# Optimization experiments

Hardware: AMD Instinct MI355X
Metric: run time of the kernel (lower is better)

The kernel has to match this reference:

```python
import math
import jax, jax.numpy as jnp
import numpy as np

D_MODEL = 1024
HEADS = 16
B, S = 4, 2048


def setup_inputs() -> dict:
    key = jax.random.key(0)
    ks = jax.random.split(key, 8)
    scale = 1.0 / math.sqrt(D_MODEL)
    return {
        "q": jax.random.normal(ks[0], (B, S, D_MODEL), dtype=jnp.float32),
        "k": jax.random.normal(ks[1], (B, S, D_MODEL), dtype=jnp.float32),
        "v": jax.random.normal(ks[2], (B, S, D_MODEL), dtype=jnp.float32),
        "mask": jax.random.randint(ks[3], (B, S), 0, 2).astype(jnp.bool_),
        "alibi_mask": jax.random.normal(ks[4], (1, HEADS, S, S), dtype=jnp.float32),
        "Wq": jax.random.normal(ks[5], (D_MODEL, D_MODEL), dtype=jnp.float32) * scale,
        "Wk": jax.random.normal(ks[6], (D_MODEL, D_MODEL), dtype=jnp.float32) * scale,
        "Wv": jax.random.normal(ks[7], (D_MODEL, D_MODEL), dtype=jnp.float32) * scale,
    }


def _split_heads(x):
    b, s, d = x.shape
    return x.reshape(b, s, HEADS, d // HEADS).transpose(0, 2, 1, 3)  # [B,H,S,hd]


def reference(q, k, v, mask, alibi_mask, Wq, Wk, Wv):
    # QKV projections (Linear, no bias)
    qh = _split_heads(q @ Wq)
    kh = _split_heads(k @ Wk)
    vh = _split_heads(v @ Wv)
    depth = qh.shape[-1]
    # naive full attention matrix [B,H,Sq,Sk]
    w = jnp.einsum("bhqd,bhkd->bhqk", qh, kh) / math.sqrt(depth)
    # mask: [B,Sk] -> [B,1,1,Sk], True = masked
    w = jnp.where(mask[:, None, None, :], -jnp.inf, w)
    w = w + alibi_mask
    a = jax.nn.softmax(w, axis=-1)  # dropout p=0 -> identity
    out = jnp.einsum("bhqk,bhkd->bhqd", a, vh)
    # combine heads -> [B,S,D]
    out = out.transpose(0, 2, 1, 3).reshape(q.shape[0], q.shape[1], -1)
    return (out, a)
```

## Files before the change

kernel.cpp:

```cpp
#include <hip/hip_runtime.h>
#include <hip/hip_bf16.h>
#include <math.h>

constexpr int B  = 4;
constexpr int S  = 2048;
constexpr int D  = 1024;
constexpr int H  = 16;
constexpr int HD = 64;
constexpr float SCALE = 0.125f;

using f32x4 = __attribute__((ext_vector_type(4))) float;
using s16x8 = __attribute__((ext_vector_type(8))) short;
using u16x8 = __attribute__((ext_vector_type(8))) unsigned short;
using u16x4 = __attribute__((ext_vector_type(4))) unsigned short;

__device__ __forceinline__ unsigned short f2bf(float f) {
    union { float f; unsigned u; } x; x.f = f;
    unsigned r = x.u + 0x7fffu + ((x.u >> 16) & 1u);
    return (unsigned short)(r >> 16);
}
__device__ __forceinline__ float bf2f(unsigned short h) {
    union { unsigned u; float f; } x; x.u = ((unsigned)h) << 16;
    return x.f;
}

#define MFMA_BF16(Af, Bf, Cf) __builtin_amdgcn_mfma_f32_16x16x32_bf16(Af, Bf, Cf, 0, 0, 0)

__global__ __launch_bounds__(256) void k_wt(const float* __restrict__ W,
                                            unsigned short* __restrict__ Wt) {
    __shared__ unsigned short T[64][68];
    const int k0 = blockIdx.x * 64, n0 = blockIdx.y * 64;
    const int t = threadIdx.x;
    {
        const int kr = t >> 4, nc4 = (t & 15) * 4;
        for (int rr = 0; rr < 4; ++rr) {
            const int kk = kr + rr * 16;
            f32x4 wv = *reinterpret_cast<const f32x4*>(&W[(size_t)(k0 + kk) * D + n0 + nc4]);
#pragma unroll
            for (int j = 0; j < 4; ++j) T[nc4 + j][kk] = f2bf(wv[j]);
        }
    }
    __syncthreads();
    {
        const int nr = t >> 4, kc4 = (t & 15) * 4;
        for (int rr = 0; rr < 4; ++rr) {
            const int nn = nr + rr * 16;
            u16x4 o;
#pragma unroll
            for (int j = 0; j < 4; ++j) o[j] = T[nn][kc4 + j];
            *reinterpret_cast<u16x4*>(&Wt[(size_t)(n0 + nn) * D + k0 + kc4]) = o;
        }
    }
}

__global__ __launch_bounds__(256) void k_proj_mfma(const float* __restrict__ X,
                                                   const unsigned short* __restrict__ Wt,
                                                   unsigned short* __restrict__ Y) {
    __shared__ alignas(16) unsigned short As[128][72];
    __shared__ alignas(16) unsigned short Bs[128][72];
    const int bm = blockIdx.y * 128, bn = blockIdx.x * 128;
    const int t = threadIdx.x, w = t >> 6, l = t & 63;
    const int wr = w >> 1, wc = w & 1;
    const int lr = l & 15, lg = l >> 4;
    f32x4 acc[4][4] = {};

    for (int k0 = 0; k0 < D; k0 += 64) {
        {
            const int c4 = (t & 15) * 4;
            int row = t >> 4;
            for (int rr = 0; rr < 8; ++rr, row += 16) {
                f32x4 xv = *reinterpret_cast<const f32x4*>(&X[(size_t)(bm + row) * D + k0 + c4]);
                u16x4 hv;
#pragma unroll
                for (int j = 0; j < 4; ++j) hv[j] = f2bf(xv[j]);
                *reinterpret_cast<u16x4*>(&As[row][c4]) = hv;
            }
        }
        for (int i = 0; i < 4; ++i) {
            const int idx = t + i * 256;
            const int row = idx >> 3, c8 = (idx & 7) * 8;
            *reinterpret_cast<u16x8*>(&Bs[row][c8]) =
                *reinterpret_cast<const u16x8*>(&Wt[(size_t)(bn + row) * D + k0 + c8]);
        }
        __syncthreads();
#pragma unroll
        for (int kk = 0; kk < 2; ++kk) {
            s16x8 af[4], bf[4];
#pragma unroll
            for (int f = 0; f < 4; ++f) {
                af[f] = *reinterpret_cast<const s16x8*>(&As[wr * 64 + f * 16 + lr][kk * 32 + lg * 8]);
                bf[f] = *reinterpret_cast<const s16x8*>(&Bs[wc * 64 + f * 16 + lr][kk * 32 + lg * 8]);
            }
#pragma unroll
            for (int fm = 0; fm < 4; ++fm)
#pragma unroll
                for (int fn = 0; fn < 4; ++fn)
                    acc[fm][fn] = MFMA_BF16(af[fm], bf[fn], acc[fm][fn]);
        }
        __syncthreads();
    }
#pragma unroll
    for (int fm = 0; fm < 4; ++fm)
#pragma unroll
        for (int fn = 0; fn < 4; ++fn)
#pragma unroll
            for (int r = 0; r < 4; ++r) {
                const int m = bm + wr * 64 + fm * 16 + lg * 4 + r;
                const int n = bn + wc * 64 + fn * 16 + lr;
                const int b = m >> 11, s = m & (S - 1);
                const int h = n >> 6, e = n & 63;
                Y[(((size_t)(b * H + h) * S) + s) * HD + e] = f2bf(acc[fm][fn][r]);
            }
}

__global__ __launch_bounds__(256) void k_vt(const unsigned short* __restrict__ Vh,
                                            unsigned short* __restrict__ VT) {
    __shared__ alignas(16) unsigned short T[64][264];
    const int bh = blockIdx.y;
    const int s0 = blockIdx.x * 256;
    const int t = threadIdx.x;
    {
        const int e4 = (t & 15) * 4;
        int sr = t >> 4;
        for (int rr = 0; rr < 16; ++rr, sr += 16) {
            u16x4 vv = *reinterpret_cast<const u16x4*>(&Vh[((size_t)bh * S + s0 + sr) * HD + e4]);
#pragma unroll
            for (int j = 0; j < 4; ++j) T[e4 + j][sr] = vv[j];
        }
    }
    __syncthreads();
    {
        const int e = t >> 2, sl0 = (t & 3) * 64;
        for (int c = 0; c < 8; ++c) {
            u16x8 o = *reinterpret_cast<const u16x8*>(&T[e][sl0 + c * 8]);
            *reinterpret_cast<u16x8*>(&VT[((size_t)bh * HD + e) * S + s0 + sl0 + c * 8]) = o;
        }
    }
}

__global__ __launch_bounds__(256) void k_abf16(const float* __restrict__ A,
                                               unsigned short* __restrict__ O) {
    const size_t N = (size_t)H * S * S;
    const size_t stride = (size_t)gridDim.x * 256 * 8;
    for (size_t i = ((size_t)blockIdx.x * 256 + threadIdx.x) * 8; i < N; i += stride) {
        f32x4 a0 = *reinterpret_cast<const f32x4*>(&A[i]);
        f32x4 a1 = *reinterpret_cast<const f32x4*>(&A[i + 4]);
        u16x8 o;
#pragma unroll
        for (int j = 0; j < 4; ++j) { o[j] = f2bf(a0[j]); o[4 + j] = f2bf(a1[j]); }
        *reinterpret_cast<u16x8*>(&O[i]) = o;
    }
}

template <bool ABF16>
__global__ __launch_bounds__(512, 4) void k_sumexp(
    const unsigned short* __restrict__ QH, const unsigned short* __restrict__ KH,
    const float* __restrict__ ALIBI, const unsigned short* __restrict__ ABF,
    const int* __restrict__ MASK, float* __restrict__ INVL) {
    __shared__ alignas(16) unsigned short Ks[64][72];
    __shared__ alignas(16) unsigned short ALs[128][72];

    const int bh = blockIdx.y, b = bh >> 4, h = bh & 15;
    const int q0 = blockIdx.x * 128;
    const int t = threadIdx.x, w = t >> 6, ln = t & 63;
    const int lr = ln & 15, lg = ln >> 4;

    const unsigned short* Qb = QH + (size_t)bh * S * HD;
    const unsigned short* Kb = KH + (size_t)bh * S * HD;
    const size_t hoff = (size_t)h * S * S;

    s16x8 qf[2];
#pragma unroll
    for (int kk = 0; kk < 2; ++kk)
        qf[kk] = *reinterpret_cast<const s16x8*>(
            &Qb[(size_t)(q0 + w * 16 + lr) * HD + kk * 32 + lg * 8]);

    float psum[4] = {0.f, 0.f, 0.f, 0.f};

    for (int k0 = 0; k0 < S; k0 += 64) {
        {
            const int row = t >> 3, c8 = (t & 7) * 8;
            *reinterpret_cast<u16x8*>(&Ks[row][c8]) =
                *reinterpret_cast<const u16x8*>(&Kb[(size_t)(k0 + row) * HD + c8]);
        }
#pragma unroll
        for (int i = 0; i < 2; ++i) {
            const int idx = t + i * 512, row = idx >> 3, c8 = (idx & 7) * 8;
            u16x8 av;
            if constexpr (ABF16) {
                av = *reinterpret_cast<const u16x8*>(&ABF[hoff + (size_t)(q0 + row) * S + k0 + c8]);
            } else {
                f32x4 a0 = *reinterpret_cast<const f32x4*>(&ALIBI[hoff + (size_t)(q0 + row) * S + k0 + c8]);
                f32x4 a1 = *reinterpret_cast<const f32x4*>(&ALIBI[hoff + (size_t)(q0 + row) * S + k0 + c8 + 4]);
#pragma unroll
                for (int j = 0; j < 4; ++j) { av[j] = f2bf(a0[j]); av[4 + j] = f2bf(a1[j]); }
            }
            *reinterpret_cast<u16x8*>(&ALs[row][c8]) = av;
        }
        float madd[4];
#pragma unroll
        for (int fn = 0; fn < 4; ++fn)
            madd[fn] = MASK[b * S + k0 + fn * 16 + lr] ? -1e30f : 0.f;
        __syncthreads();

        f32x4 acc[4] = {};
#pragma unroll
        for (int kk = 0; kk < 2; ++kk)
#pragma unroll
            for (int fn = 0; fn < 4; ++fn) {
                s16x8 kf = *reinterpret_cast<const s16x8*>(&Ks[fn * 16 + lr][kk * 32 + lg * 8]);
                acc[fn] = MFMA_BF16(qf[kk], kf, acc[fn]);
            }
#pragma unroll
        for (int r = 0; r < 4; ++r) {
            const int rowl = w * 16 + lg * 4 + r;
            float s = 0.f;
#pragma unroll
            for (int fn = 0; fn < 4; ++fn)
                s += __expf(fmaf(acc[fn][r], SCALE, bf2f(ALs[rowl][fn * 16 + lr]) + madd[fn]));
            psum[r] += s;
        }
        __syncthreads();
    }

#pragma unroll
    for (int r = 0; r < 4; ++r) {
        float ps = psum[r];
#pragma unroll
        for (int off = 1; off < 16; off <<= 1) ps += __shfl_xor(ps, off, 64);
        if (lr == 0)
            INVL[(size_t)bh * S + q0 + w * 16 + lg * 4 + r] = 1.0f / ps;
    }
}

template <bool ABF16>
__global__ __launch_bounds__(512, 2) void k_attn(
    const unsigned short* __restrict__ QH, const unsigned short* __restrict__ KH,
    const unsigned short* __restrict__ VT, const float* __restrict__ ALIBI,
    const unsigned short* __restrict__ ABF, const int* __restrict__ MASK,
    const float* __restrict__ INVL, float* __restrict__ Aout,
    float* __restrict__ OUT) {
    __shared__ alignas(16) unsigned short Ps[128][72];
    __shared__ alignas(16) unsigned short Ks[64][72];
    __shared__ alignas(16) unsigned short Vs[64][72];
    __shared__ alignas(16) unsigned short ALs[128][72];

    const int bh = blockIdx.y, b = bh >> 4, h = bh & 15;
    const int q0 = blockIdx.x * 128;
    const int t = threadIdx.x, w = t >> 6, ln = t & 63;
    const int lr = ln & 15, lg = ln >> 4;

    const unsigned short* Qb = QH + (size_t)bh * S * HD;
    const unsigned short* Kb = KH + (size_t)bh * S * HD;
    const unsigned short* Vb = VT + (size_t)bh * HD * S;
    const size_t hoff = (size_t)h * S * S;

    s16x8 qf[2];
#pragma unroll
    for (int kk = 0; kk < 2; ++kk)
        qf[kk] = *reinterpret_cast<const s16x8*>(
            &Qb[(size_t)(q0 + w * 16 + lr) * HD + kk * 32 + lg * 8]);

    float invl[4];
#pragma unroll
    for (int r = 0; r < 4; ++r)
        invl[r] = INVL[(size_t)bh * S + q0 + w * 16 + lg * 4 + r];

    f32x4 oacc[4] = {};
    for (int k0 = 0; k0 < S; k0 += 64) {
        {
            const int row = t >> 3, c8 = (t & 7) * 8;
            *reinterpret_cast<u16x8*>(&Ks[row][c8]) =
                *reinterpret_cast<const u16x8*>(&Kb[(size_t)(k0 + row) * HD + c8]);
            *reinterpret_cast<u16x8*>(&Vs[row][c8]) =
                *reinterpret_cast<const u16x8*>(&Vb[(size_t)row * S + k0 + c8]);
        }
#pragma unroll
        for (int i = 0; i < 2; ++i) {
            const int idx = t + i * 512, row = idx >> 3, c8 = (idx & 7) * 8;
            u16x8 av;
            if constexpr (ABF16) {
                av = *reinterpret_cast<const u16x8*>(&ABF[hoff + (size_t)(q0 + row) * S + k0 + c8]);
            } else {
                f32x4 a0 = *reinterpret_cast<const f32x4*>(&ALIBI[hoff + (size_t)(q0 + row) * S + k0 + c8]);
                f32x4 a1 = *reinterpret_cast<const f32x4*>(&ALIBI[hoff + (size_t)(q0 + row) * S + k0 + c8 + 4]);
#pragma unroll
                for (int j = 0; j < 4; ++j) { av[j] = f2bf(a0[j]); av[4 + j] = f2bf(a1[j]); }
            }
            *reinterpret_cast<u16x8*>(&ALs[row][c8]) = av;
        }
        float madd[4];
#pragma unroll
        for (int fn = 0; fn < 4; ++fn)
            madd[fn] = MASK[b * S + k0 + fn * 16 + lr] ? -1e30f : 0.f;
        __syncthreads();

        f32x4 acc[4] = {};
#pragma unroll
        for (int kk = 0; kk < 2; ++kk)
#pragma unroll
            for (int fn = 0; fn < 4; ++fn) {
                s16x8 kf = *reinterpret_cast<const s16x8*>(&Ks[fn * 16 + lr][kk * 32 + lg * 8]);
                acc[fn] = MFMA_BF16(qf[kk], kf, acc[fn]);
            }
#pragma unroll
        for (int r = 0; r < 4; ++r) {
            const int rowl = w * 16 + lg * 4 + r;
#pragma unroll
            for (int fn = 0; fn < 4; ++fn) {
                float p = __expf(fmaf(acc[fn][r], SCALE,
                                      bf2f(ALs[rowl][fn * 16 + lr]) + madd[fn])) * invl[r];
                Ps[rowl][fn * 16 + lr] = f2bf(p);
            }
        }
        __syncthreads();

#pragma unroll
        for (int i = 0; i < 2; ++i) {
            const int idx = t + i * 512, row = idx >> 3, sub = idx & 7;
            u16x8 pv = *reinterpret_cast<const u16x8*>(&Ps[row][sub * 8]);
            f32x4 o0, o1;
#pragma unroll
            for (int j = 0; j < 4; ++j) { o0[j] = bf2f(pv[j]); o1[j] = bf2f(pv[4 + j]); }
            float* dst = &Aout[((size_t)bh * S + q0 + row) * S + k0 + sub * 8];
            *reinterpret_cast<f32x4*>(dst) = o0;
            *reinterpret_cast<f32x4*>(dst + 4) = o1;
        }
#pragma unroll
        for (int c = 0; c < 2; ++c) {
            s16x8 pa = *reinterpret_cast<const s16x8*>(&Ps[w * 16 + lr][c * 32 + lg * 8]);
#pragma unroll
            for (int fn = 0; fn < 4; ++fn) {
                s16x8 vf = *reinterpret_cast<const s16x8*>(&Vs[fn * 16 + lr][c * 32 + lg * 8]);
                oacc[fn] = MFMA_BF16(pa, vf, oacc[fn]);
            }
        }
        __syncthreads();
    }

#pragma unroll
    for (int fn = 0; fn < 4; ++fn)
#pragma unroll
        for (int r = 0; r < 4; ++r)
            OUT[(size_t)(b * S + q0 + w * 16 + lg * 4 + r) * D + h * HD + fn * 16 + lr] =
                oacc[fn][r];
}

extern "C" void kernel_launch(void* const* d_in, const int* in_sizes, int n_in,
                              void* d_out, int out_size, void* d_ws, size_t ws_size,
                              hipStream_t stream) {
    const float* q     = (const float*)d_in[0];
    const float* k     = (const float*)d_in[1];
    const float* v     = (const float*)d_in[2];
    const int*   mask  = (const int*)d_in[3];
    const float* alibi = (const float*)d_in[4];
    const float* Wq    = (const float*)d_in[5];
    const float* Wk    = (const float*)d_in[6];
    const float* Wv    = (const float*)d_in[7];

    float* out = (float*)d_out;
    float* a   = out + (size_t)B * S * D;

    const size_t NH = (size_t)B * H * S * HD;
    unsigned short* qh  = (unsigned short*)d_ws;
    unsigned short* kh  = qh + NH;
    unsigned short* vh  = kh + NH;
    unsigned short* vT  = vh + NH;
    unsigned short* wqt = vT + NH;
    unsigned short* wkt = wqt + (size_t)D * D;
    unsigned short* wvt = wkt + (size_t)D * D;
    float*          invl = (float*)(wvt + (size_t)D * D);
    unsigned short* abf  = (unsigned short*)(invl + (size_t)B * H * S);

    const size_t need_bf16 =
        ((size_t)((unsigned short*)abf - qh) + (size_t)H * S * S) * sizeof(unsigned short);
    const bool use_abf16 = ws_size >= need_bf16;

    const dim3 blk(256);

    k_wt<<<dim3(D / 64, D / 64), blk, 0, stream>>>(Wq, wqt);
    k_wt<<<dim3(D / 64, D / 64), blk, 0, stream>>>(Wk, wkt);
    k_wt<<<dim3(D / 64, D / 64), blk, 0, stream>>>(Wv, wvt);

    if (use_abf16)
        k_abf16<<<dim3(8192), blk, 0, stream>>>(alibi, abf);

    k_proj_mfma<<<dim3(D / 128, (B * S) / 128), blk, 0, stream>>>(q, wqt, qh);
    k_proj_mfma<<<dim3(D / 128, (B * S) / 128), blk, 0, stream>>>(k, wkt, kh);
    k_proj_mfma<<<dim3(D / 128, (B * S) / 128), blk, 0, stream>>>(v, wvt, vh);

    k_vt<<<dim3(S / 256, B * H), blk, 0, stream>>>(vh, vT);

    if (use_abf16) {
        k_sumexp<true><<<dim3(S / 128, B * H), dim3(512), 0, stream>>>(
            qh, kh, alibi, abf, mask, invl);
        k_attn<true><<<dim3(S / 128, B * H), dim3(512), 0, stream>>>(
            qh, kh, vT, alibi, abf, mask, invl, a, out);
    } else {
        k_sumexp<false><<<dim3(S / 128, B * H), dim3(512), 0, stream>>>(
            qh, kh, alibi, abf, mask, invl);
        k_attn<false><<<dim3(S / 128, B * H), dim3(512), 0, stream>>>(
            qh, kh, vT, alibi, abf, mask, invl, a, out);
    }
}
```

Measured before the change: 714.3 us.

## Fuse V transpose into projection, swap MFMA operands, write probabilities directly

Merges the V projection with its transpose into one kernel that writes V^T through shared memory, which removes a separate pass and an intermediate buffer. In the sumexp and attn kernels the MFMA operands are swapped so each lane holds four consecutive keys of one query row. This lets the attention probabilities go straight from registers to global memory with nontemporal f32x4 stores, replacing the earlier shared-memory staging pass. The mask is folded into the bf16 alibi tile, and exp is replaced with exp2 using log2e-prescaled constants. The attn occupancy hint rises from 2 to 4 blocks per SM, which risks register pressure.

```diff
diff --git a/kernel.cpp b/kernel.cpp
--- a/kernel.cpp
+++ b/kernel.cpp
@@ -7,7 +7,8 @@
 constexpr int D  = 1024;
 constexpr int H  = 16;
 constexpr int HD = 64;
-constexpr float SCALE = 0.125f;
+constexpr float LOG2E  = 1.4426950408889634f;
+constexpr float SCALE2 = 0.125f * LOG2E;
 
 using f32x4 = __attribute__((ext_vector_type(4))) float;
 using s16x8 = __attribute__((ext_vector_type(8))) short;
@@ -19,9 +20,20 @@
     unsigned r = x.u + 0x7fffu + ((x.u >> 16) & 1u);
     return (unsigned short)(r >> 16);
 }
+__device__ __forceinline__ unsigned short f2bf_fast(float f) {
+    union { float f; unsigned u; } x; x.f = f;
+    return (unsigned short)((x.u + 0x8000u) >> 16);
+}
 __device__ __forceinline__ float bf2f(unsigned short h) {
     union { unsigned u; float f; } x; x.u = ((unsigned)h) << 16;
     return x.f;
+}
+__device__ __forceinline__ float fexp2(float x) {
+#if __has_builtin(__builtin_amdgcn_exp2f)
+    return __builtin_amdgcn_exp2f(x);
+#else
+    return __expf(x * 0.6931471805599453f);
+#endif
 }
 
 #define MFMA_BF16(Af, Bf, Cf) __builtin_amdgcn_mfma_f32_16x16x32_bf16(Af, Bf, Cf, 0, 0, 0)
@@ -113,28 +125,69 @@
             }
 }
 
-__global__ __launch_bounds__(256) void k_vt(const unsigned short* __restrict__ Vh,
-                                            unsigned short* __restrict__ VT) {
-    __shared__ alignas(16) unsigned short T[64][264];
-    const int bh = blockIdx.y;
-    const int s0 = blockIdx.x * 256;
-    const int t = threadIdx.x;
-    {
-        const int e4 = (t & 15) * 4;
-        int sr = t >> 4;
-        for (int rr = 0; rr < 16; ++rr, sr += 16) {
-            u16x4 vv = *reinterpret_cast<const u16x4*>(&Vh[((size_t)bh * S + s0 + sr) * HD + e4]);
-#pragma unroll
-            for (int j = 0; j < 4; ++j) T[e4 + j][sr] = vv[j];
-        }
-    }
+__global__ __launch_bounds__(256) void k_projv_mfma(const float* __restrict__ X,
+                                                    const unsigned short* __restrict__ Wt,
+                                                    unsigned short* __restrict__ VT) {
+    __shared__ alignas(16) unsigned short SM[2][128][72];
+    unsigned short (*As)[72] = SM[0];
+    unsigned short (*Bs)[72] = SM[1];
+    const int bm = blockIdx.y * 128, bn = blockIdx.x * 128;
+    const int t = threadIdx.x, w = t >> 6, l = t & 63;
+    const int wr = w >> 1, wc = w & 1;
+    const int lr = l & 15, lg = l >> 4;
+    f32x4 acc[4][4] = {};
+
+    for (int k0 = 0; k0 < D; k0 += 64) {
+        {
+            const int c4 = (t & 15) * 4;
+            int row = t >> 4;
+            for (int rr = 0; rr < 8; ++rr, row += 16) {
+                f32x4 xv = *reinterpret_cast<const f32x4*>(&X[(size_t)(bm + row) * D + k0 + c4]);
+                u16x4 hv;
+#pragma unroll
+                for (int j = 0; j < 4; ++j) hv[j] = f2bf(xv[j]);
+                *reinterpret_cast<u16x4*>(&As[row][c4]) = hv;
+            }
+        }
+        for (int i = 0; i < 4; ++i) {
+            const int idx = t + i * 256;
+            const int row = idx >> 3, c8 = (idx & 7) * 8;
+            *reinterpret_cast<u16x8*>(&Bs[row][c8]) =
+                *reinterpret_cast<const u16x8*>(&Wt[(size_t)(bn + row) * D + k0 + c8]);
+        }
+        __syncthreads();
+#pragma unroll
+        for (int kk = 0; kk < 2; ++kk) {
+            s16x8 af[4], bf[4];
+#pragma unroll
+            for (int f = 0; f < 4; ++f) {
+                af[f] = *reinterpret_cast<const s16x8*>(&As[wr * 64 + f * 16 + lr][kk * 32 + lg * 8]);
+                bf[f] = *reinterpret_cast<const s16x8*>(&Bs[wc * 64 + f * 16 + lr][kk * 32 + lg * 8]);
+            }
+#pragma unroll
+            for (int fm = 0; fm < 4; ++fm)
+#pragma unroll
+                for (int fn = 0; fn < 4; ++fn)
+                    acc[fm][fn] = MFMA_BF16(af[fm], bf[fn], acc[fm][fn]);
+        }
+        __syncthreads();
+    }
+    unsigned short (*T)[144] = reinterpret_cast<unsigned short(*)[144]>(&SM[0][0][0]);
+#pragma unroll
+    for (int fm = 0; fm < 4; ++fm)
+#pragma unroll
+        for (int fn = 0; fn < 4; ++fn)
+#pragma unroll
+            for (int r = 0; r < 4; ++r)
+                T[wc * 64 + fn * 16 + lr][wr * 64 + fm * 16 + lg * 4 + r] = f2bf(acc[fm][fn][r]);
     __syncthreads();
-    {
-        const int e = t >> 2, sl0 = (t & 3) * 64;
-        for (int c = 0; c < 8; ++c) {
-            u16x8 o = *reinterpret_cast<const u16x8*>(&T[e][sl0 + c * 8]);
-            *reinterpret_cast<u16x8*>(&VT[((size_t)bh * HD + e) * S + s0 + sl0 + c * 8]) = o;
-        }
+    const int b = bm >> 11, s0 = bm & (S - 1);
+    for (int it = 0; it < 8; ++it) {
+        const int idx = t + it * 256;
+        const int row = idx >> 4, c8 = (idx & 15) * 8;
+        const int h = (bn + row) >> 6, e = (bn + row) & 63;
+        *reinterpret_cast<u16x8*>(&VT[((size_t)(b * H + h) * HD + e) * S + s0 + c8]) =
+            *reinterpret_cast<const u16x8*>(&T[row][c8]);
     }
 }
 
@@ -147,7 +200,10 @@
         f32x4 a1 = *reinterpret_cast<const f32x4*>(&A[i + 4]);
         u16x8 o;
 #pragma unroll
-        for (int j = 0; j < 4; ++j) { o[j] = f2bf(a0[j]); o[4 + j] = f2bf(a1[j]); }
+        for (int j = 0; j < 4; ++j) {
+            o[j]     = f2bf(a0[j] * LOG2E);
+            o[4 + j] = f2bf(a1[j] * LOG2E);
+        }
         *reinterpret_cast<u16x8*>(&O[i]) = o;
     }
 }
@@ -164,18 +220,18 @@
     const int q0 = blockIdx.x * 128;
     const int t = threadIdx.x, w = t >> 6, ln = t & 63;
     const int lr = ln & 15, lg = ln >> 4;
-
-    const unsigned short* Qb = QH + (size_t)bh * S * HD;
+    const unsigned short NEGBIG = f2bf(-1e30f);
+    const size_t hoff = (size_t)h * S * S;
+
     const unsigned short* Kb = KH + (size_t)bh * S * HD;
-    const size_t hoff = (size_t)h * S * S;
 
     s16x8 qf[2];
 #pragma unroll
     for (int kk = 0; kk < 2; ++kk)
         qf[kk] = *reinterpret_cast<const s16x8*>(
-            &Qb[(size_t)(q0 + w * 16 + lr) * HD + kk * 32 + lg * 8]);
-
-    float psum[4] = {0.f, 0.f, 0.f, 0.f};
+            &QH[((size_t)bh * S + q0 + w * 16 + lr) * HD + kk * 32 + lg * 8]);
+
+    float psum = 0.f;
 
     for (int k0 = 0; k0 < S; k0 += 64) {
         {
@@ -186,6 +242,8 @@
 #pragma unroll
         for (int i = 0; i < 2; ++i) {
             const int idx = t + i * 512, row = idx >> 3, c8 = (idx & 7) * 8;
+            int4 m0 = *reinterpret_cast<const int4*>(&MASK[b * S + k0 + c8]);
+            int4 m1 = *reinterpret_cast<const int4*>(&MASK[b * S + k0 + c8 + 4]);
             u16x8 av;
             if constexpr (ABF16) {
                 av = *reinterpret_cast<const u16x8*>(&ABF[hoff + (size_t)(q0 + row) * S + k0 + c8]);
@@ -193,14 +251,22 @@
                 f32x4 a0 = *reinterpret_cast<const f32x4*>(&ALIBI[hoff + (size_t)(q0 + row) * S + k0 + c8]);
                 f32x4 a1 = *reinterpret_cast<const f32x4*>(&ALIBI[hoff + (size_t)(q0 + row) * S + k0 + c8 + 4]);
 #pragma unroll
-                for (int j = 0; j < 4; ++j) { av[j] = f2bf(a0[j]); av[4 + j] = f2bf(a1[j]); }
-            }
-            *reinterpret_cast<u16x8*>(&ALs[row][c8]) = av;
-        }
-        float madd[4];
-#pragma unroll
-        for (int fn = 0; fn < 4; ++fn)
-            madd[fn] = MASK[b * S + k0 + fn * 16 + lr] ? -1e30f : 0.f;
+                for (int j = 0; j < 4; ++j) {
+                    av[j] = f2bf(a0[j] * LOG2E);
+                    av[4 + j] = f2bf(a1[j] * LOG2E);
+                }
+            }
+            u16x8 sv;
+            sv[0] = m0.x ? NEGBIG : av[0];
+            sv[1] = m0.y ? NEGBIG : av[1];
+            sv[2] = m0.z ? NEGBIG : av[2];
+            sv[3] = m0.w ? NEGBIG : av[3];
+            sv[4] = m1.x ? NEGBIG : av[4];
+            sv[5] = m1.y ? NEGBIG : av[5];
+            sv[6] = m1.z ? NEGBIG : av[6];
+            sv[7] = m1.w ? NEGBIG : av[7];
+            *reinterpret_cast<u16x8*>(&ALs[row][c8]) = sv;
+        }
         __syncthreads();
 
         f32x4 acc[4] = {};
@@ -209,64 +275,59 @@
 #pragma unroll
             for (int fn = 0; fn < 4; ++fn) {
                 s16x8 kf = *reinterpret_cast<const s16x8*>(&Ks[fn * 16 + lr][kk * 32 + lg * 8]);
-                acc[fn] = MFMA_BF16(qf[kk], kf, acc[fn]);
-            }
-#pragma unroll
-        for (int r = 0; r < 4; ++r) {
-            const int rowl = w * 16 + lg * 4 + r;
-            float s = 0.f;
-#pragma unroll
-            for (int fn = 0; fn < 4; ++fn)
-                s += __expf(fmaf(acc[fn][r], SCALE, bf2f(ALs[rowl][fn * 16 + lr]) + madd[fn]));
-            psum[r] += s;
-        }
-        __syncthreads();
-    }
-
-#pragma unroll
-    for (int r = 0; r < 4; ++r) {
-        float ps = psum[r];
-#pragma unroll
-        for (int off = 1; off < 16; off <<= 1) ps += __shfl_xor(ps, off, 64);
-        if (lr == 0)
-            INVL[(size_t)bh * S + q0 + w * 16 + lg * 4 + r] = 1.0f / ps;
-    }
+                acc[fn] = MFMA_BF16(kf, qf[kk], acc[fn]);
+            }
+#pragma unroll
+        for (int fn = 0; fn < 4; ++fn) {
+            u16x4 alv = *reinterpret_cast<const u16x4*>(&ALs[w * 16 + lr][fn * 16 + lg * 4]);
+            f32x4 al;
+#pragma unroll
+            for (int j = 0; j < 4; ++j) al[j] = bf2f(alv[j]);
+            f32x4 sv = acc[fn] * SCALE2 + al;
+            psum += fexp2(sv[0]) + fexp2(sv[1]) + fexp2(sv[2]) + fexp2(sv[3]);
+        }
+        __syncthreads();
+    }
+
+    psum += __shfl_xor(psum, 16, 64);
+    psum += __shfl_xor(psum, 32, 64);
+    if (lg == 0)
+        INVL[(size_t)bh * S + q0 + w * 16 + lr] = 1.0f / psum;
 }
 
 template <bool ABF16>
-__global__ __launch_bounds__(512, 2) void k_attn(
+__global__ __launch_bounds__(512, 4) void k_attn(
     const unsigned short* __restrict__ QH, const unsigned short* __restrict__ KH,
     const unsigned short* __restrict__ VT, const float* __restrict__ ALIBI,
     const unsigned short* __restrict__ ABF, const int* __restrict__ MASK,
     const float* __restrict__ INVL, float* __restrict__ Aout,
     float* __restrict__ OUT) {
-    __shared__ alignas(16) unsigned short Ps[128][72];
     __shared__ alignas(16) unsigned short Ks[64][72];
     __shared__ alignas(16) unsigned short Vs[64][72];
     __shared__ alignas(16) unsigned short ALs[128][72];
+    __shared__ alignas(16) unsigned short Ps[128][72];
 
     const int bh = blockIdx.y, b = bh >> 4, h = bh & 15;
     const int q0 = blockIdx.x * 128;
     const int t = threadIdx.x, w = t >> 6, ln = t & 63;
     const int lr = ln & 15, lg = ln >> 4;
-
-    const unsigned short* Qb = QH + (size_t)bh * S * HD;
+    const unsigned short NEGBIG = f2bf(-1e30f);
+    const size_t hoff = (size_t)h * S * S;
+
     const unsigned short* Kb = KH + (size_t)bh * S * HD;
     const unsigned short* Vb = VT + (size_t)bh * HD * S;
-    const size_t hoff = (size_t)h * S * S;
 
     s16x8 qf[2];
 #pragma unroll
     for (int kk = 0; kk < 2; ++kk)
         qf[kk] = *reinterpret_cast<const s16x8*>(
-            &Qb[(size_t)(q0 + w * 16 + lr) * HD + kk * 32 + lg * 8]);
-
-    float invl[4];
-#pragma unroll
-    for (int r = 0; r < 4; ++r)
-        invl[r] = INVL[(size_t)bh * S + q0 + w * 16 + lg * 4 + r];
+            &QH[((size_t)bh * S + q0 + w * 16 + lr) * HD + kk * 32 + lg * 8]);
+
+    const float invl = INVL[(size_t)bh * S + q0 + w * 16 + lr];
+    float* arow = Aout + ((size_t)bh * S + q0 + w * 16 + lr) * S;
 
     f32x4 oacc[4] = {};
+
     for (int k0 = 0; k0 < S; k0 += 64) {
         {
             const int row = t >> 3, c8 = (t & 7) * 8;
@@ -278,6 +339,8 @@
 #pragma unroll
         for (int i = 0; i < 2; ++i) {
             const int idx = t + i * 512, row = idx >> 3, c8 = (idx & 7) * 8;
+            int4 m0 = *reinterpret_cast<const int4*>(&MASK[b * S + k0 + c8]);
+            int4 m1 = *reinterpret_cast<const int4*>(&MASK[b * S + k0 + c8 + 4]);
             u16x8 av;
             if constexpr (ABF16) {
                 av = *reinterpret_cast<const u16x8*>(&ABF[hoff + (size_t)(q0 + row) * S + k0 + c8]);
@@ -285,14 +348,22 @@
                 f32x4 a0 = *reinterpret_cast<const f32x4*>(&ALIBI[hoff + (size_t)(q0 + row) * S + k0 + c8]);
                 f32x4 a1 = *reinterpret_cast<const f32x4*>(&ALIBI[hoff + (size_t)(q0 + row) * S + k0 + c8 + 4]);
 #pragma unroll
-                for (int j = 0; j < 4; ++j) { av[j] = f2bf(a0[j]); av[4 + j] = f2bf(a1[j]); }
-            }
-            *reinterpret_cast<u16x8*>(&ALs[row][c8]) = av;
-        }
-        float madd[4];
-#pragma unroll
-        for (int fn = 0; fn < 4; ++fn)
-            madd[fn] = MASK[b * S + k0 + fn * 16 + lr] ? -1e30f : 0.f;
+                for (int j = 0; j < 4; ++j) {
+                    av[j] = f2bf(a0[j] * LOG2E);
+                    av[4 + j] = f2bf(a1[j] * LOG2E);
+                }
+            }
+            u16x8 sv;
+            sv[0] = m0.x ? NEGBIG : av[0];
+            sv[1] = m0.y ? NEGBIG : av[1];
+            sv[2] = m0.z ? NEGBIG : av[2];
+            sv[3] = m0.w ? NEGBIG : av[3];
+            sv[4] = m1.x ? NEGBIG : av[4];
+            sv[5] = m1.y ? NEGBIG : av[5];
+            sv[6] = m1.z ? NEGBIG : av[6];
+            sv[7] = m1.w ? NEGBIG : av[7];
+            *reinterpret_cast<u16x8*>(&ALs[row][c8]) = sv;
+        }
         __syncthreads();
 
         f32x4 acc[4] = {};
@@ -301,31 +372,28 @@
 #pragma unroll
             for (int fn = 0; fn < 4; ++fn) {
                 s16x8 kf = *reinterpret_cast<const s16x8*>(&Ks[fn * 16 + lr][kk * 32 + lg * 8]);
-                acc[fn] = MFMA_BF16(qf[kk], kf, acc[fn]);
-            }
-#pragma unroll
-        for (int r = 0; r < 4; ++r) {
-            const int rowl = w * 16 + lg * 4 + r;
-#pragma unroll
-            for (int fn = 0; fn < 4; ++fn) {
-                float p = __expf(fmaf(acc[fn][r], SCALE,
-                                      bf2f(ALs[rowl][fn * 16 + lr]) + madd[fn])) * invl[r];
-                Ps[rowl][fn * 16 + lr] = f2bf(p);
-            }
-        }
-        __syncthreads();
-
-#pragma unroll
-        for (int i = 0; i < 2; ++i) {
-            const int idx = t + i * 512, row = idx >> 3, sub = idx & 7;
-            u16x8 pv = *reinterpret_cast<const u16x8*>(&Ps[row][sub * 8]);
-            f32x4 o0, o1;
-#pragma unroll
-            for (int j = 0; j < 4; ++j) { o0[j] = bf2f(pv[j]); o1[j] = bf2f(pv[4 + j]); }
-            float* dst = &Aout[((size_t)bh * S + q0 + row) * S + k0 + sub * 8];
-            *reinterpret_cast<f32x4*>(dst) = o0;
-            *reinterpret_cast<f32x4*>(dst + 4) = o1;
-        }
+                acc[fn] = MFMA_BF16(kf, qf[kk], acc[fn]);
+            }
+
+#pragma unroll
+        for (int fn = 0; fn < 4; ++fn) {
+            u16x4 alv = *reinterpret_cast<const u16x4*>(&ALs[w * 16 + lr][fn * 16 + lg * 4]);
+            f32x4 al;
+#pragma unroll
+            for (int j = 0; j < 4; ++j) al[j] = bf2f(alv[j]);
+            f32x4 sv = acc[fn] * SCALE2 + al;
+            f32x4 p;
+#pragma unroll
+            for (int j = 0; j < 4; ++j) p[j] = fexp2(sv[j]);
+            p *= invl;
+            __builtin_nontemporal_store(
+                p, reinterpret_cast<f32x4*>(arow + k0 + fn * 16 + lg * 4));
+            u16x4 pb;
+#pragma unroll
+            for (int j = 0; j < 4; ++j) pb[j] = f2bf_fast(p[j]);
+            *reinterpret_cast<u16x4*>(&Ps[w * 16 + lr][fn * 16 + lg * 4]) = pb;
+        }
+
 #pragma unroll
         for (int c = 0; c < 2; ++c) {
             s16x8 pa = *reinterpret_cast<const s16x8*>(&Ps[w * 16 + lr][c * 32 + lg * 8]);
@@ -364,8 +432,7 @@
     const size_t NH = (size_t)B * H * S * HD;
     unsigned short* qh  = (unsigned short*)d_ws;
     unsigned short* kh  = qh + NH;
-    unsigned short* vh  = kh + NH;
-    unsigned short* vT  = vh + NH;
+    unsigned short* vT  = kh + NH;
     unsigned short* wqt = vT + NH;
     unsigned short* wkt = wqt + (size_t)D * D;
     unsigned short* wvt = wkt + (size_t)D * D;
@@ -373,7 +440,7 @@
     unsigned short* abf  = (unsigned short*)(invl + (size_t)B * H * S);
 
     const size_t need_bf16 =
-        ((size_t)((unsigned short*)abf - qh) + (size_t)H * S * S) * sizeof(unsigned short);
+        ((size_t)(abf - qh) + (size_t)H * S * S) * sizeof(unsigned short);
     const bool use_abf16 = ws_size >= need_bf16;
 
     const dim3 blk(256);
@@ -387,9 +454,7 @@
 
     k_proj_mfma<<<dim3(D / 128, (B * S) / 128), blk, 0, stream>>>(q, wqt, qh);
     k_proj_mfma<<<dim3(D / 128, (B * S) / 128), blk, 0, stream>>>(k, wkt, kh);
-    k_proj_mfma<<<dim3(D / 128, (B * S) / 128), blk, 0, stream>>>(v, wvt, vh);
-
-    k_vt<<<dim3(S / 256, B * H), blk, 0, stream>>>(vh, vT);
+    k_projv_mfma<<<dim3(D / 128, (B * S) / 128), blk, 0, stream>>>(v, wvt, vT);
 
     if (use_abf16) {
         k_sumexp<true><<<dim3(S / 128, B * H), dim3(512), 0, stream>>>(
```

After: 700.7 us. About the same (-1.9%).
